# Optimization experiments

Measured on AMD Instinct MI355X. Metric: run time of the kernel, lower is better.

Reference implementation:

```python
import jax, jax.numpy as jnp
import numpy as np

N, B, LMAX, DIM, IMG_DIM, LY, H = 32768, 16, 2560, 512, 768, 256, 8


def _layernorm(x, g, b, eps=1e-5):
    mu = jnp.mean(x, axis=-1, keepdims=True)
    var = jnp.mean(jnp.square(x - mu), axis=-1, keepdims=True)
    return (x - mu) * jax.lax.rsqrt(var + eps) * g + b


def setup_inputs() -> dict:
    key = jax.random.key(0)
    ks = jax.random.split(key, 16)
    s = DIM ** -0.5
    # ragged per-batch counts summing to N, all <= LMAX
    counts = np.full(B, N // B, dtype=np.int64)
    counts[: B // 2] += 200
    counts[B // 2:] -= 200
    batch_ids = jnp.asarray(np.repeat(np.arange(B), counts), dtype=jnp.int32)
    return {
        "F": jax.random.normal(ks[0], (N, DIM), jnp.float32),
        "y": jax.random.normal(ks[1], (B, LY, IMG_DIM), jnp.float32),
        "ln_g": jnp.ones((DIM,), jnp.float32),
        "ln_b": jnp.zeros((DIM,), jnp.float32),
        "Wq": jax.random.normal(ks[2], (DIM, DIM), jnp.float32) * s,
        "Wk": jax.random.normal(ks[3], (DIM, DIM), jnp.float32) * s,
        "Wv": jax.random.normal(ks[4], (DIM, DIM), jnp.float32) * s,
        "bq": jnp.zeros((DIM,), jnp.float32),
        "bk": jnp.zeros((DIM,), jnp.float32),
        "bv": jnp.zeros((DIM,), jnp.float32),
        "Wo": jax.random.normal(ks[5], (DIM, DIM), jnp.float32) * s,
        "bo": jnp.zeros((DIM,), jnp.float32),
        "W1": jax.random.normal(ks[6], (DIM, IMG_DIM), jnp.float32) * (IMG_DIM ** -0.5),
        "b1": jnp.zeros((DIM,), jnp.float32),
        "W2": jax.random.normal(ks[7], (DIM, DIM), jnp.float32) * s,
        "b2": jnp.zeros((DIM,), jnp.float32),
        "batch_ids": batch_ids,
        "Lmax": LMAX,
    }


def reference(F, y, ln_g, ln_b, Wq, Wk, Wv, bq, bk, bv, Wo, bo, W1, b1, W2, b2, batch_ids, Lmax):
    Bb, Ly, _ = y.shape
    n, dim = F.shape
    dh = dim // H
    # sparse -> dense: per-token slot index within its batch (batch_ids sorted)
    offsets = jnp.searchsorted(batch_ids, jnp.arange(Bb, dtype=batch_ids.dtype))
    pos = jnp.arange(n, dtype=jnp.int32) - offsets[batch_ids].astype(jnp.int32)
    xd = jnp.zeros((Bb, Lmax, dim), F.dtype).at[batch_ids, pos].set(F)  # [B,Lmax,D]
    # NOTE: self.norm is re-bound in subclass => same LayerNorm used twice
    xd = _layernorm(xd, ln_g, ln_b)
    # MLP fuse of image features: Linear -> GELU(exact) -> Linear
    ym = jax.nn.gelu(y @ W1.T + b1, approximate=False) @ W2.T + b2  # [B,Ly,D]
    # MHA cross-attention (no key_padding_mask: mask arg defaults to None)
    q = (xd @ Wq.T + bq).reshape(Bb, Lmax, H, dh)
    k = (ym @ Wk.T + bk).reshape(Bb, Ly, H, dh)
    v = (ym @ Wv.T + bv).reshape(Bb, Ly, H, dh)
    scores = jnp.einsum("bqhd,bkhd->bhqk", q, k) * (dh ** -0.5)
    attn = jax.nn.softmax(scores, axis=-1)
    o = jnp.einsum("bhqk,bkhd->bqhd", attn, v).reshape(Bb, Lmax, dim)
    o = o @ Wo.T + bo
    out_dense = _layernorm(xd + o, ln_g, ln_b)
    # dense -> sparse gather (equivalent to x_dense[x_mask])
    return out_dense[batch_ids, pos]
```

## Files before the change

kernel.cpp:

```cpp
#include <hip/hip_runtime.h>
#include <stdint.h>

#define NTOK 32768
#define BD   512
#define NB   16
#define LYK  256
#define IMGD 768

typedef __attribute__((ext_vector_type(4))) float f32x4;
typedef __attribute__((ext_vector_type(8))) short s16x8;
typedef __attribute__((ext_vector_type(4))) unsigned short u16x4;
typedef unsigned short u16;

__device__ __forceinline__ float bf2f(u16 u) {
  union { uint32_t i; float f; } v; v.i = ((uint32_t)u) << 16; return v.f;
}
__device__ __forceinline__ u16 f2bf(float f) {
  union { float f; uint32_t i; } v; v.f = f;
  uint32_t r = v.i + 0x7fffu + ((v.i >> 16) & 1u);
  return (u16)(r >> 16);
}
__device__ __forceinline__ u16 f2bf_fast(float f) {
  union { float f; uint32_t i; } v; v.f = f;
  return (u16)((v.i + 0x8000u) >> 16);
}
__device__ __forceinline__ void gl_lds16(const u16* g, u16* l) {
  __builtin_amdgcn_global_load_lds(
      (const __attribute__((address_space(1))) uint32_t*)g,
      (__attribute__((address_space(3))) uint32_t*)l, 16, 0, 0);
}
__device__ __forceinline__ f32x4 mfma16(s16x8 a, s16x8 b, f32x4 c) {
  return __builtin_amdgcn_mfma_f32_16x16x32_bf16(a, b, c, 0, 0, 0);
}
__device__ __forceinline__ uint32_t cvtpk(float a, float b) {
  uint32_t r;
  asm("v_cvt_pk_bf16_f32 %0, %1, %2" : "=v"(r) : "v"(a), "v"(b));
  return r;
}

__global__ __launch_bounds__(256) void prep(
    const float* __restrict__ wq, const float* __restrict__ wk,
    const float* __restrict__ wv, const float* __restrict__ wo,
    const float* __restrict__ w2, const float* __restrict__ w1,
    const float* __restrict__ y,  const float* __restrict__ F,
    const float* __restrict__ g,  const float* __restrict__ be,
    const int* __restrict__ bids,
    u16* __restrict__ dq, u16* __restrict__ dkv, u16* __restrict__ dwo,
    u16* __restrict__ dw2, u16* __restrict__ dw1, u16* __restrict__ dy,
    u16* __restrict__ xn, int* __restrict__ off) {
  const int bid = blockIdx.x;
  if (bid < 2368) {
    const float* s; u16* d; int base;
    if      (bid < 128)  { s = wq; d = dq;            base = 0;   }
    else if (bid < 256)  { s = wk; d = dkv;           base = 128; }
    else if (bid < 384)  { s = wv; d = dkv + 262144;  base = 256; }
    else if (bid < 512)  { s = wo; d = dwo;           base = 384; }
    else if (bid < 640)  { s = w2; d = dw2;           base = 512; }
    else if (bid < 832)  { s = w1; d = dw1;           base = 640; }
    else                 { s = y;  d = dy;            base = 832; }
    int i = ((bid - base) * 256 + threadIdx.x) * 8;
    f32x4 a = *(const f32x4*)(s + i);
    f32x4 b = *(const f32x4*)(s + i + 4);
    s16x8 o;
#pragma unroll
    for (int j = 0; j < 4; ++j) { o[j] = (short)f2bf(a[j]); o[4 + j] = (short)f2bf(b[j]); }
    *(s16x8*)(d + i) = o;
  } else if (bid < 10560) {
    const int lane = threadIdx.x & 63;
    const size_t row = (size_t)(bid - 2368) * 4 + (threadIdx.x >> 6);
    const float* x = F + row * BD + lane * 8;
    f32x4 a = *(const f32x4*)x;
    f32x4 b = *(const f32x4*)(x + 4);
    float v[8] = {a[0], a[1], a[2], a[3], b[0], b[1], b[2], b[3]};
    float s = 0.f, s2 = 0.f;
#pragma unroll
    for (int j = 0; j < 8; ++j) { s += v[j]; s2 += v[j] * v[j]; }
#pragma unroll
    for (int m = 1; m < 64; m <<= 1) { s += __shfl_xor(s, m); s2 += __shfl_xor(s2, m); }
    float mean = s * (1.f / BD);
    float rstd = rsqrtf(s2 * (1.f / BD) - mean * mean + 1e-5f);
    const float* gp = g + lane * 8;
    const float* bp = be + lane * 8;
    s16x8 o;
#pragma unroll
    for (int j = 0; j < 8; ++j) o[j] = (short)f2bf((v[j] - mean) * rstd * gp[j] + bp[j]);
    *(s16x8*)(xn + row * BD + lane * 8) = o;
  } else {
    int b = threadIdx.x;
    if (b > NB) return;
    int lo = 0, hi = NTOK;
    while (lo < hi) { int mid = (lo + hi) >> 1; if (bids[mid] < b) lo = mid + 1; else hi = mid; }
    off[b] = lo;
  }
}

__global__ __launch_bounds__(256) void ln_bf16_f32(const u16* __restrict__ Z,
                                                   const float* __restrict__ g,
                                                   const float* __restrict__ be,
                                                   float* __restrict__ out) {
  const int lane = threadIdx.x & 63;
  const size_t row = (size_t)blockIdx.x * 4 + (threadIdx.x >> 6);
  s16x8 zv = *(const s16x8*)(Z + row * BD + lane * 8);
  float v[8];
#pragma unroll
  for (int j = 0; j < 8; ++j) v[j] = bf2f((u16)zv[j]);
  float s = 0.f, s2 = 0.f;
#pragma unroll
  for (int j = 0; j < 8; ++j) { s += v[j]; s2 += v[j] * v[j]; }
#pragma unroll
  for (int m = 1; m < 64; m <<= 1) { s += __shfl_xor(s, m); s2 += __shfl_xor(s2, m); }
  float mean = s * (1.f / BD);
  float rstd = rsqrtf(s2 * (1.f / BD) - mean * mean + 1e-5f);
  const float* gp = g + lane * 8;
  const float* bp = be + lane * 8;
  f32x4 o0, o1;
#pragma unroll
  for (int j = 0; j < 4; ++j) o0[j] = (v[j] - mean) * rstd * gp[j] + bp[j];
#pragma unroll
  for (int j = 0; j < 4; ++j) o1[j] = (v[4 + j] - mean) * rstd * gp[4 + j] + bp[4 + j];
  float* op = out + row * BD + lane * 8;
  *(f32x4*)op = o0;
  *(f32x4*)(op + 4) = o1;
}

template <int EPI>
__global__ __launch_bounds__(256, 2) void gemm64(const u16* __restrict__ A,
                                                 const u16* __restrict__ W,
                                                 const float* __restrict__ bias,
                                                 u16* __restrict__ C, int K) {
  __shared__ u16 As[64 * 32];
  __shared__ u16 Bs[128 * 32];
  const int tid = threadIdx.x;
  const int wave = tid >> 6, lane = tid & 63;
  const int wn = wave * 32;
  const int quad = lane >> 4, l16 = lane & 15;
  const int m0 = blockIdx.x * 64, n0 = blockIdx.y * 128;

  f32x4 acc[4][2];
#pragma unroll
  for (int i = 0; i < 4; ++i)
#pragma unroll
    for (int j = 0; j < 2; ++j) acc[i][j] = f32x4{0.f, 0.f, 0.f, 0.f};

  const int scol = (lane & 3) * 8;
  const u16* gA0 = A + (size_t)(m0 + wave * 16 + (lane >> 2)) * K + scol;
  const u16* gW0 = W + (size_t)(n0 + wave * 32 + (lane >> 2)) * K + scol;
  const u16* gW1 = gW0 + (size_t)16 * K;
  u16* lA = As + wave * 512;
  u16* lB = Bs + wave * 1024;

  for (int k0 = 0; k0 < K; k0 += 32) {
    __syncthreads();
    gl_lds16(gA0 + k0, lA);
    gl_lds16(gW0 + k0, lB);
    gl_lds16(gW1 + k0, lB + 512);
    __syncthreads();
    s16x8 af[4], bfr[2];
#pragma unroll
    for (int mt = 0; mt < 4; ++mt)
      af[mt] = *(const s16x8*)&As[(mt * 16 + l16) * 32 + quad * 8];
#pragma unroll
    for (int nt = 0; nt < 2; ++nt)
      bfr[nt] = *(const s16x8*)&Bs[(wn + nt * 16 + l16) * 32 + quad * 8];
#pragma unroll
    for (int mt = 0; mt < 4; ++mt)
#pragma unroll
      for (int nt = 0; nt < 2; ++nt)
        acc[mt][nt] = mfma16(af[mt], bfr[nt], acc[mt][nt]);
  }

#pragma unroll
  for (int nt = 0; nt < 2; ++nt) {
    const int n = n0 + wn + nt * 16 + l16;
    const float bia = bias[n];
#pragma unroll
    for (int mt = 0; mt < 4; ++mt) {
      const int mb = m0 + mt * 16 + quad * 4;
#pragma unroll
      for (int r = 0; r < 4; ++r) {
        float v = acc[mt][nt][r] + bia;
        if (EPI == 1) v = 0.5f * v * (1.f + erff(v * 0.70710678118654752f));
        C[(size_t)(mb + r) * BD + n] = f2bf(v);
      }
    }
  }
}

template <int EPI, int SWZ>
__global__ __launch_bounds__(256, 2) void gemm128(const u16* __restrict__ A,
                                                  const u16* __restrict__ W,
                                                  const float* __restrict__ bias,
                                                  u16* __restrict__ C,
                                                  const u16* __restrict__ resid,
                                                  u16* __restrict__ C2,
                                                  const float* __restrict__ bias2,
                                                  int K) {
  __shared__ u16 As[2][128 * 32];
  __shared__ u16 Bs[2][128 * 32];
  const int tid = threadIdx.x;
  const int wave = tid >> 6, lane = tid & 63;
  const int wm = (wave & 1) * 64, wn = (wave >> 1) * 64;
  const int quad = lane >> 4, l16 = lane & 15;
  int m_t, n_t;
  if (SWZ) {
    const int bid = blockIdx.x;
    const int xcd = bid & 7, j = bid >> 3;
    n_t = j & 3;
    m_t = xcd + (j >> 2) * 8;
  } else {
    m_t = blockIdx.x; n_t = blockIdx.y;
  }
  const int m0 = m_t * 128, n0 = n_t * 128;

  f32x4 acc[4][4];
#pragma unroll
  for (int i = 0; i < 4; ++i)
#pragma unroll
    for (int j = 0; j < 4; ++j) acc[i][j] = f32x4{0.f, 0.f, 0.f, 0.f};

  const int srow = wave * 32 + (lane >> 2);
  const int scol = (lane & 3) * 8;
  const u16* gA0 = A + (size_t)(m0 + srow) * K + scol;
  const u16* gA1 = gA0 + (size_t)16 * K;
  const u16* gW0 = W + (size_t)(n0 + srow) * K + scol;
  const u16* gW1 = gW0 + (size_t)16 * K;
  const int wb = wave * 1024;

  gl_lds16(gA0, &As[0][wb]);
  gl_lds16(gA1, &As[0][wb + 512]);
  gl_lds16(gW0, &Bs[0][wb]);
  gl_lds16(gW1, &Bs[0][wb + 512]);

  int buf = 0;
  for (int k0 = 0; k0 < K; k0 += 32, buf ^= 1) {
    __syncthreads();
    if (k0 + 32 < K) {
      const int nb = buf ^ 1, k1 = k0 + 32;
      gl_lds16(gA0 + k1, &As[nb][wb]);
      gl_lds16(gA1 + k1, &As[nb][wb + 512]);
      gl_lds16(gW0 + k1, &Bs[nb][wb]);
      gl_lds16(gW1 + k1, &Bs[nb][wb + 512]);
    }
    s16x8 af[4], bfr[4];
#pragma unroll
    for (int mt = 0; mt < 4; ++mt)
      af[mt] = *(const s16x8*)&As[buf][(wm + mt * 16 + l16) * 32 + quad * 8];
#pragma unroll
    for (int nt = 0; nt < 4; ++nt)
      bfr[nt] = *(const s16x8*)&Bs[buf][(wn + nt * 16 + l16) * 32 + quad * 8];
#pragma unroll
    for (int mt = 0; mt < 4; ++mt)
#pragma unroll
      for (int nt = 0; nt < 4; ++nt)
        acc[mt][nt] = mfma16(af[mt], bfr[nt], acc[mt][nt]);
  }

#pragma unroll
  for (int nt = 0; nt < 4; ++nt) {
    const int n = n0 + wn + nt * 16 + l16;
    const float bia = (EPI == 3) ? (n < BD ? bias[n] : bias2[n - BD]) : bias[n];
#pragma unroll
    for (int mt = 0; mt < 4; ++mt) {
      const int mb = m0 + wm + mt * 16 + quad * 4;
      if (EPI == 3 && n >= BD) {
        u16x4 pk;
#pragma unroll
        for (int r = 0; r < 4; ++r) pk[r] = f2bf(acc[mt][nt][r] + bia);
        const int b = mb >> 8, k0i = mb & 255;
        *(u16x4*)&C2[((size_t)b * BD + (n - BD)) * LYK + k0i] = pk;
      } else {
#pragma unroll
        for (int r = 0; r < 4; ++r) {
          float v = acc[mt][nt][r] + bia;
          size_t idx = (size_t)(mb + r) * BD + n;
          if (EPI == 2) v += bf2f(resid[idx]);
          C[idx] = f2bf(v);
        }
      }
    }
  }
}

__global__ __launch_bounds__(512, 1) void attn_k(const u16* __restrict__ Q,
                                                 const u16* __restrict__ Kg,
                                                 const u16* __restrict__ VT,
                                                 const int* __restrict__ off,
                                                 u16* __restrict__ O) {
  const int bid = blockIdx.x;
  const int lin = (bid & 7) * 64 + (bid >> 3);
  const int t = lin & 3;
  const int h = (lin >> 2) & 7;
  const int b = lin >> 5;

  __shared__ u16 KS[256 * 64];
  __shared__ u16 VS[64 * 256];
  __shared__ u16 P[128 * 264];

  const int tid = threadIdx.x;
  const int wave = tid >> 6, lane = tid & 63;
  const int quad = lane >> 4, l16 = lane & 15;

  {
    const int c8 = lane & 7, r8 = lane >> 3;
    const u16* kbase = Kg + (size_t)(b * LYK) * BD + h * 64 + ((c8 ^ r8) << 3);
#pragma unroll
    for (int j = 0; j < 4; ++j) {
      const int blk = wave * 4 + j;
      gl_lds16(kbase + (size_t)(blk * 8 + r8) * BD, KS + blk * 512);
    }
    const int c32 = lane & 31, r2 = lane >> 5;
#pragma unroll
    for (int j = 0; j < 4; ++j) {
      const int blk = wave * 4 + j;
      const int r = blk * 2 + r2;
      gl_lds16(VT + (size_t)(b * BD + h * 64 + r) * LYK + ((c32 ^ (r & 31)) << 3),
               VS + blk * 512);
    }
  }
  __syncthreads();

  const int qbase = off[b], qend = off[b + 1];
  const int kc0 = ((quad ^ (l16 & 7)) << 3);
  const int kc1 = (((quad + 4) ^ (l16 & 7)) << 3);
  const int prow = (wave * 16 + l16) * 264;
  int vbase[4], vm[4];
#pragma unroll
  for (int n2 = 0; n2 < 4; ++n2) {
    const int rv = n2 * 16 + l16;
    vbase[n2] = rv * 256;
    vm[n2] = (rv & 31) << 3;
  }

  for (int it = t;; it += 4) {
    const int q0 = qbase + it * 128;
    if (q0 >= qend) break;
    const int qw = q0 + wave * 16;
    if (qw >= qend) continue;
    int qrow = qw + l16;
    if (qrow > qend - 1) qrow = qend - 1;
    const u16* qp = Q + (size_t)qrow * BD + h * 64 + quad * 8;
    const s16x8 aq0 = *(const s16x8*)qp;
    const s16x8 aq1 = *(const s16x8*)(qp + 32);

    f32x4 sacc[16];
#pragma unroll
    for (int nt = 0; nt < 16; ++nt) sacc[nt] = f32x4{0.f, 0.f, 0.f, 0.f};
#pragma unroll
    for (int nt = 0; nt < 16; ++nt) {
      const u16* kp = &KS[(nt * 16 + l16) * 64];
      const s16x8 k0 = *(const s16x8*)(kp + kc0);
      const s16x8 k1 = *(const s16x8*)(kp + kc1);
      sacc[nt] = mfma16(k0, aq0, sacc[nt]);
      sacc[nt] = mfma16(k1, aq1, sacc[nt]);
    }

    f32x4 m4 = sacc[0];
#pragma unroll
    for (int nt = 1; nt < 16; ++nt)
#pragma unroll
      for (int r = 0; r < 4; ++r) m4[r] = fmaxf(m4[r], sacc[nt][r]);
    float mx = fmaxf(fmaxf(m4[0], m4[1]), fmaxf(m4[2], m4[3]));
    mx = fmaxf(mx, __shfl_xor(mx, 16));
    mx = fmaxf(mx, __shfl_xor(mx, 32));
    const float c1 = 0.18033688011112042f;
    const float mc = -mx * c1;
    f32x4 s4 = f32x4{0.f, 0.f, 0.f, 0.f};
#pragma unroll
    for (int nt = 0; nt < 16; ++nt)
#pragma unroll
      for (int r = 0; r < 4; ++r) {
        const float p = __builtin_exp2f(fmaf(sacc[nt][r], c1, mc));
        sacc[nt][r] = p;
        s4[r] += p;
      }
    float sum = (s4[0] + s4[1]) + (s4[2] + s4[3]);
    sum += __shfl_xor(sum, 16);
    sum += __shfl_xor(sum, 32);
    const float inv = 1.f / sum;

#pragma unroll
    for (int nt = 0; nt < 16; ++nt) {
      uint2 pk;
      pk.x = cvtpk(sacc[nt][0], sacc[nt][1]);
      pk.y = cvtpk(sacc[nt][2], sacc[nt][3]);
      *(uint2*)&P[prow + nt * 16 + quad * 4] = pk;
    }

    f32x4 oacc[4];
#pragma unroll
    for (int n2 = 0; n2 < 4; ++n2) oacc[n2] = f32x4{0.f, 0.f, 0.f, 0.f};
#pragma unroll
    for (int kc = 0; kc < 8; ++kc) {
      const s16x8 ap = *(const s16x8*)&P[prow + kc * 32 + quad * 8];
#pragma unroll
      for (int n2 = 0; n2 < 4; ++n2) {
        const s16x8 bv = *(const s16x8*)&VS[vbase[n2] + ((kc * 32 + quad * 8) ^ vm[n2])];
        oacc[n2] = mfma16(ap, bv, oacc[n2]);
      }
    }

    float invr[4];
#pragma unroll
    for (int r = 0; r < 4; ++r) invr[r] = __shfl(inv, quad * 4 + r);
#pragma unroll
    for (int n2 = 0; n2 < 4; ++n2)
#pragma unroll
      for (int r = 0; r < 4; ++r) {
        const int q = qw + quad * 4 + r;
        if (q < qend)
          O[(size_t)q * BD + h * 64 + n2 * 16 + l16] = f2bf(oacc[n2][r] * invr[r]);
      }
  }
}

extern "C" void kernel_launch(void* const* d_in, const int* in_sizes, int n_in,
                              void* d_out, int out_size, void* d_ws, size_t ws_size,
                              hipStream_t stream) {
  const float* F    = (const float*)d_in[0];
  const float* yIn  = (const float*)d_in[1];
  const float* ln_g = (const float*)d_in[2];
  const float* ln_b = (const float*)d_in[3];
  const float* Wq   = (const float*)d_in[4];
  const float* Wk   = (const float*)d_in[5];
  const float* Wv   = (const float*)d_in[6];
  const float* bq   = (const float*)d_in[7];
  const float* bk   = (const float*)d_in[8];
  const float* bv   = (const float*)d_in[9];
  const float* Wo   = (const float*)d_in[10];
  const float* bo   = (const float*)d_in[11];
  const float* W1   = (const float*)d_in[12];
  const float* b1   = (const float*)d_in[13];
  const float* W2   = (const float*)d_in[14];
  const float* b2   = (const float*)d_in[15];
  const int* bids   = (const int*)d_in[16];

  char* ws = (char*)d_ws;
  size_t cur = 0;
  auto alloc = [&](size_t bytes) {
    void* p = ws + cur;
    cur += (bytes + 255) & ~(size_t)255;
    return p;
  };

  int* off   = (int*)alloc(68);
  u16* wq_b  = (u16*)alloc((size_t)262144 * 2);
  u16* wkv_b = (u16*)alloc((size_t)524288 * 2);
  u16* wo_b  = (u16*)alloc((size_t)262144 * 2);
  u16* w2_b  = (u16*)alloc((size_t)262144 * 2);
  u16* w1_b  = (u16*)alloc((size_t)393216 * 2);
  u16* y_b   = (u16*)alloc((size_t)3145728 * 2);
  u16* U     = (u16*)alloc((size_t)4096 * BD * 2);
  u16* ym    = (u16*)alloc((size_t)4096 * BD * 2);
  u16* Kb    = (u16*)alloc((size_t)4096 * BD * 2);
  u16* VT    = (u16*)alloc((size_t)NB * BD * LYK * 2);
  u16* xn    = (u16*)alloc((size_t)NTOK * BD * 2);
  u16* Qb    = (u16*)alloc((size_t)NTOK * BD * 2);
  u16* Ob    = (u16*)alloc((size_t)NTOK * BD * 2);
  u16* Zb    = (u16*)alloc((size_t)NTOK * BD * 2);

  prep<<<10561, 256, 0, stream>>>(Wq, Wk, Wv, Wo, W2, W1, yIn, F, ln_g, ln_b, bids,
                                  wq_b, wkv_b, wo_b, w2_b, w1_b, y_b, xn, off);

  gemm64<1><<<dim3(64, 4), 256, 0, stream>>>(y_b, w1_b, b1, U, IMGD);
  gemm64<0><<<dim3(64, 4), 256, 0, stream>>>(U, w2_b, b2, ym, BD);
  gemm128<3, 0><<<dim3(32, 8), 256, 0, stream>>>(ym, wkv_b, bk, Kb, nullptr, VT, bv, BD);
  gemm128<0, 1><<<1024, 256, 0, stream>>>(xn, wq_b, bq, Qb, nullptr, nullptr, nullptr, BD);
  attn_k<<<512, 512, 0, stream>>>(Qb, Kb, VT, off, Ob);
  gemm128<2, 1><<<1024, 256, 0, stream>>>(Ob, wo_b, bo, Zb, xn, nullptr, nullptr, BD);
  ln_bf16_f32<<<NTOK / 4, 256, 0, stream>>>(Zb, ln_g, ln_b, (float*)d_out);
}
```

Baseline: 339.8 us.

## Keep softmax probabilities in registers via permlane swaps instead of LDS round-trip

```diff
diff --git a/kernel.cpp b/kernel.cpp
--- a/kernel.cpp
+++ b/kernel.cpp
@@ -10,6 +10,7 @@
 typedef __attribute__((ext_vector_type(4))) float f32x4;
 typedef __attribute__((ext_vector_type(8))) short s16x8;
 typedef __attribute__((ext_vector_type(4))) unsigned short u16x4;
+typedef __attribute__((ext_vector_type(4))) int i32x4;
 typedef unsigned short u16;
 
 __device__ __forceinline__ float bf2f(u16 u) {
@@ -19,10 +20,6 @@
   union { float f; uint32_t i; } v; v.f = f;
   uint32_t r = v.i + 0x7fffu + ((v.i >> 16) & 1u);
   return (u16)(r >> 16);
-}
-__device__ __forceinline__ u16 f2bf_fast(float f) {
-  union { float f; uint32_t i; } v; v.f = f;
-  return (u16)((v.i + 0x8000u) >> 16);
 }
 __device__ __forceinline__ void gl_lds16(const u16* g, u16* l) {
   __builtin_amdgcn_global_load_lds(
@@ -281,7 +278,7 @@
   }
 }
 
-__global__ __launch_bounds__(512, 1) void attn_k(const u16* __restrict__ Q,
+__global__ __launch_bounds__(512, 4) void attn_k(const u16* __restrict__ Q,
                                                  const u16* __restrict__ Kg,
                                                  const u16* __restrict__ VT,
                                                  const int* __restrict__ off,
@@ -294,7 +291,6 @@
 
   __shared__ u16 KS[256 * 64];
   __shared__ u16 VS[64 * 256];
-  __shared__ u16 P[128 * 264];
 
   const int tid = threadIdx.x;
   const int wave = tid >> 6, lane = tid & 63;
@@ -322,7 +318,6 @@
   const int qbase = off[b], qend = off[b + 1];
   const int kc0 = ((quad ^ (l16 & 7)) << 3);
   const int kc1 = (((quad + 4) ^ (l16 & 7)) << 3);
-  const int prow = (wave * 16 + l16) * 264;
   int vbase[4], vm[4];
 #pragma unroll
   for (int n2 = 0; n2 < 4; ++n2) {
@@ -364,34 +359,38 @@
     mx = fmaxf(mx, __shfl_xor(mx, 32));
     const float c1 = 0.18033688011112042f;
     const float mc = -mx * c1;
+
     f32x4 s4 = f32x4{0.f, 0.f, 0.f, 0.f};
-#pragma unroll
-    for (int nt = 0; nt < 16; ++nt)
-#pragma unroll
-      for (int r = 0; r < 4; ++r) {
-        const float p = __builtin_exp2f(fmaf(sacc[nt][r], c1, mc));
-        sacc[nt][r] = p;
-        s4[r] += p;
-      }
+    uint32_t pk[32];
+#pragma unroll
+    for (int nt = 0; nt < 16; ++nt) {
+      const float p0 = __builtin_exp2f(fmaf(sacc[nt][0], c1, mc));
+      const float p1 = __builtin_exp2f(fmaf(sacc[nt][1], c1, mc));
+      const float p2 = __builtin_exp2f(fmaf(sacc[nt][2], c1, mc));
+      const float p3 = __builtin_exp2f(fmaf(sacc[nt][3], c1, mc));
+      s4[0] += p0; s4[1] += p1; s4[2] += p2; s4[3] += p3;
+      pk[2 * nt]     = cvtpk(p0, p1);
+      pk[2 * nt + 1] = cvtpk(p2, p3);
+    }
     float sum = (s4[0] + s4[1]) + (s4[2] + s4[3]);
     sum += __shfl_xor(sum, 16);
     sum += __shfl_xor(sum, 32);
     const float inv = 1.f / sum;
 
-#pragma unroll
-    for (int nt = 0; nt < 16; ++nt) {
-      uint2 pk;
-      pk.x = cvtpk(sacc[nt][0], sacc[nt][1]);
-      pk.y = cvtpk(sacc[nt][2], sacc[nt][3]);
-      *(uint2*)&P[prow + nt * 16 + quad * 4] = pk;
-    }
-
     f32x4 oacc[4];
 #pragma unroll
     for (int n2 = 0; n2 < 4; ++n2) oacc[n2] = f32x4{0.f, 0.f, 0.f, 0.f};
 #pragma unroll
     for (int kc = 0; kc < 8; ++kc) {
-      const s16x8 ap = *(const s16x8*)&P[prow + kc * 32 + quad * 8];
+      uint32_t x0 = pk[4 * kc],     y0 = pk[4 * kc + 2];
+      uint32_t x1 = pk[4 * kc + 1], y1 = pk[4 * kc + 3];
+      asm("v_permlane32_swap_b32 %0, %1" : "+v"(x0), "+v"(y0));
+      asm("v_permlane16_swap_b32 %0, %1" : "+v"(x0), "+v"(y0));
+      asm("v_permlane32_swap_b32 %0, %1" : "+v"(x1), "+v"(y1));
+      asm("v_permlane16_swap_b32 %0, %1" : "+v"(x1), "+v"(y1));
+      i32x4 aw;
+      aw[0] = (int)x0; aw[1] = (int)x1; aw[2] = (int)y0; aw[3] = (int)y1;
+      const s16x8 ap = __builtin_bit_cast(s16x8, aw);
 #pragma unroll
       for (int n2 = 0; n2 < 4; ++n2) {
         const s16x8 bv = *(const s16x8*)&VS[vbase[n2] + ((kc * 32 + quad * 8) ^ vm[n2])];
```

Measured after the change: 338.4 us. Within noise of the previous version (-0.4%).

## Rewrite attention kernel with 32x32 MFMA and register-resident probabilities

Applied to the files above, without the earlier changes.

```diff
diff --git a/kernel.cpp b/kernel.cpp
--- a/kernel.cpp
+++ b/kernel.cpp
@@ -8,8 +8,10 @@
 #define IMGD 768
 
 typedef __attribute__((ext_vector_type(4))) float f32x4;
+typedef __attribute__((ext_vector_type(16))) float f32x16;
 typedef __attribute__((ext_vector_type(8))) short s16x8;
 typedef __attribute__((ext_vector_type(4))) unsigned short u16x4;
+typedef __attribute__((ext_vector_type(4))) int i32x4;
 typedef unsigned short u16;
 
 __device__ __forceinline__ float bf2f(u16 u) {
@@ -20,10 +22,6 @@
   uint32_t r = v.i + 0x7fffu + ((v.i >> 16) & 1u);
   return (u16)(r >> 16);
 }
-__device__ __forceinline__ u16 f2bf_fast(float f) {
-  union { float f; uint32_t i; } v; v.f = f;
-  return (u16)((v.i + 0x8000u) >> 16);
-}
 __device__ __forceinline__ void gl_lds16(const u16* g, u16* l) {
   __builtin_amdgcn_global_load_lds(
       (const __attribute__((address_space(1))) uint32_t*)g,
@@ -31,6 +29,9 @@
 }
 __device__ __forceinline__ f32x4 mfma16(s16x8 a, s16x8 b, f32x4 c) {
   return __builtin_amdgcn_mfma_f32_16x16x32_bf16(a, b, c, 0, 0, 0);
+}
+__device__ __forceinline__ f32x16 mfma32(s16x8 a, s16x8 b, f32x16 c) {
+  return __builtin_amdgcn_mfma_f32_32x32x16_bf16(a, b, c, 0, 0, 0);
 }
 __device__ __forceinline__ uint32_t cvtpk(float a, float b) {
   uint32_t r;
@@ -281,37 +282,35 @@
   }
 }
 
-__global__ __launch_bounds__(512, 1) void attn_k(const u16* __restrict__ Q,
+__global__ __launch_bounds__(256, 2) void attn_k(const u16* __restrict__ Q,
                                                  const u16* __restrict__ Kg,
                                                  const u16* __restrict__ VT,
                                                  const int* __restrict__ off,
                                                  u16* __restrict__ O) {
-  const int bid = blockIdx.x;
-  const int lin = (bid & 7) * 64 + (bid >> 3);
-  const int t = lin & 3;
-  const int h = (lin >> 2) & 7;
-  const int b = lin >> 5;
+  const int chunk = blockIdx.x, h = blockIdx.y, b = blockIdx.z;
+  const int qbase = off[b], qend = off[b + 1];
+  const int q0 = qbase + chunk * 128;
+  if (q0 >= qend) return;
 
   __shared__ u16 KS[256 * 64];
   __shared__ u16 VS[64 * 256];
-  __shared__ u16 P[128 * 264];
 
   const int tid = threadIdx.x;
   const int wave = tid >> 6, lane = tid & 63;
-  const int quad = lane >> 4, l16 = lane & 15;
+  const int l32 = lane & 31, hi = lane >> 5;
 
   {
     const int c8 = lane & 7, r8 = lane >> 3;
     const u16* kbase = Kg + (size_t)(b * LYK) * BD + h * 64 + ((c8 ^ r8) << 3);
 #pragma unroll
-    for (int j = 0; j < 4; ++j) {
-      const int blk = wave * 4 + j;
+    for (int j = 0; j < 8; ++j) {
+      const int blk = wave * 8 + j;
       gl_lds16(kbase + (size_t)(blk * 8 + r8) * BD, KS + blk * 512);
     }
     const int c32 = lane & 31, r2 = lane >> 5;
 #pragma unroll
-    for (int j = 0; j < 4; ++j) {
-      const int blk = wave * 4 + j;
+    for (int j = 0; j < 8; ++j) {
+      const int blk = wave * 8 + j;
       const int r = blk * 2 + r2;
       gl_lds16(VT + (size_t)(b * BD + h * 64 + r) * LYK + ((c32 ^ (r & 31)) << 3),
                VS + blk * 512);
@@ -319,97 +318,105 @@
   }
   __syncthreads();
 
-  const int qbase = off[b], qend = off[b + 1];
-  const int kc0 = ((quad ^ (l16 & 7)) << 3);
-  const int kc1 = (((quad + 4) ^ (l16 & 7)) << 3);
-  const int prow = (wave * 16 + l16) * 264;
-  int vbase[4], vm[4];
-#pragma unroll
-  for (int n2 = 0; n2 < 4; ++n2) {
-    const int rv = n2 * 16 + l16;
-    vbase[n2] = rv * 256;
-    vm[n2] = (rv & 31) << 3;
-  }
-
-  for (int it = t;; it += 4) {
-    const int q0 = qbase + it * 128;
-    if (q0 >= qend) break;
-    const int qw = q0 + wave * 16;
-    if (qw >= qend) continue;
-    int qrow = qw + l16;
-    if (qrow > qend - 1) qrow = qend - 1;
-    const u16* qp = Q + (size_t)qrow * BD + h * 64 + quad * 8;
-    const s16x8 aq0 = *(const s16x8*)qp;
-    const s16x8 aq1 = *(const s16x8*)(qp + 32);
-
-    f32x4 sacc[16];
-#pragma unroll
-    for (int nt = 0; nt < 16; ++nt) sacc[nt] = f32x4{0.f, 0.f, 0.f, 0.f};
-#pragma unroll
-    for (int nt = 0; nt < 16; ++nt) {
-      const u16* kp = &KS[(nt * 16 + l16) * 64];
-      const s16x8 k0 = *(const s16x8*)(kp + kc0);
-      const s16x8 k1 = *(const s16x8*)(kp + kc1);
-      sacc[nt] = mfma16(k0, aq0, sacc[nt]);
-      sacc[nt] = mfma16(k1, aq1, sacc[nt]);
-    }
-
-    f32x4 m4 = sacc[0];
-#pragma unroll
-    for (int nt = 1; nt < 16; ++nt)
-#pragma unroll
-      for (int r = 0; r < 4; ++r) m4[r] = fmaxf(m4[r], sacc[nt][r]);
-    float mx = fmaxf(fmaxf(m4[0], m4[1]), fmaxf(m4[2], m4[3]));
-    mx = fmaxf(mx, __shfl_xor(mx, 16));
-    mx = fmaxf(mx, __shfl_xor(mx, 32));
-    const float c1 = 0.18033688011112042f;
-    const float mc = -mx * c1;
-    f32x4 s4 = f32x4{0.f, 0.f, 0.f, 0.f};
-#pragma unroll
-    for (int nt = 0; nt < 16; ++nt)
-#pragma unroll
-      for (int r = 0; r < 4; ++r) {
-        const float p = __builtin_exp2f(fmaf(sacc[nt][r], c1, mc));
-        sacc[nt][r] = p;
-        s4[r] += p;
+  const int qw = q0 + wave * 32;
+  if (qw >= qend) return;
+
+  int qrow = qw + l32;
+  if (qrow > qend - 1) qrow = qend - 1;
+  const u16* qp = Q + (size_t)qrow * BD + h * 64 + hi * 8;
+  s16x8 bq[4];
+#pragma unroll
+  for (int kk = 0; kk < 4; ++kk) bq[kk] = *(const s16x8*)(qp + kk * 16);
+
+  f32x16 sacc[8];
+#pragma unroll
+  for (int kt = 0; kt < 8; ++kt)
+#pragma unroll
+    for (int r = 0; r < 16; ++r) sacc[kt][r] = 0.f;
+#pragma unroll
+  for (int kt = 0; kt < 8; ++kt) {
+    const int krow = kt * 32 + l32;
+    const u16* kp = &KS[krow * 64];
+#pragma unroll
+    for (int kk = 0; kk < 4; ++kk) {
+      const int c = kk * 2 + hi;
+      const s16x8 ka = *(const s16x8*)(kp + ((c ^ (krow & 7)) << 3));
+      sacc[kt] = mfma32(ka, bq[kk], sacc[kt]);
+    }
+  }
+
+  f32x16 m16 = sacc[0];
+#pragma unroll
+  for (int kt = 1; kt < 8; ++kt)
+#pragma unroll
+    for (int r = 0; r < 16; ++r) m16[r] = fmaxf(m16[r], sacc[kt][r]);
+#pragma unroll
+  for (int r = 0; r < 8; ++r) m16[r] = fmaxf(m16[r], m16[r + 8]);
+#pragma unroll
+  for (int r = 0; r < 4; ++r) m16[r] = fmaxf(m16[r], m16[r + 4]);
+  float mx = fmaxf(fmaxf(m16[0], m16[1]), fmaxf(m16[2], m16[3]));
+  mx = fmaxf(mx, __shfl_xor(mx, 32));
+  const float c1 = 0.18033688011112042f;
+  const float mc = -mx * c1;
+
+  f32x16 ssum;
+#pragma unroll
+  for (int r = 0; r < 16; ++r) ssum[r] = 0.f;
+#pragma unroll
+  for (int kt = 0; kt < 8; ++kt)
+#pragma unroll
+    for (int r = 0; r < 16; ++r) {
+      const float p = __builtin_exp2f(fmaf(sacc[kt][r], c1, mc));
+      sacc[kt][r] = p;
+      ssum[r] += p;
+    }
+#pragma unroll
+  for (int r = 0; r < 8; ++r) ssum[r] += ssum[r + 8];
+#pragma unroll
+  for (int r = 0; r < 4; ++r) ssum[r] += ssum[r + 4];
+  float sum = (ssum[0] + ssum[1]) + (ssum[2] + ssum[3]);
+  sum += __shfl_xor(sum, 32);
+  const float inv = 1.f / sum;
+
+  f32x16 oacc0, oacc1;
+#pragma unroll
+  for (int r = 0; r < 16; ++r) { oacc0[r] = 0.f; oacc1[r] = 0.f; }
+#pragma unroll
+  for (int kt = 0; kt < 8; ++kt) {
+    uint32_t pk[8];
+#pragma unroll
+    for (int j = 0; j < 8; ++j)
+      pk[j] = cvtpk(sacc[kt][2 * j] * inv, sacc[kt][2 * j + 1] * inv);
+    asm("v_permlane32_swap_b32 %0, %1" : "+v"(pk[0]), "+v"(pk[2]));
+    asm("v_permlane32_swap_b32 %0, %1" : "+v"(pk[1]), "+v"(pk[3]));
+    asm("v_permlane32_swap_b32 %0, %1" : "+v"(pk[4]), "+v"(pk[6]));
+    asm("v_permlane32_swap_b32 %0, %1" : "+v"(pk[5]), "+v"(pk[7]));
+#pragma unroll
+    for (int kc = 0; kc < 2; ++kc) {
+      i32x4 aw;
+      aw[0] = (int)pk[4 * kc];     aw[1] = (int)pk[4 * kc + 1];
+      aw[2] = (int)pk[4 * kc + 2]; aw[3] = (int)pk[4 * kc + 3];
+      const s16x8 ap = __builtin_bit_cast(s16x8, aw);
+      const int c = kt * 4 + kc * 2 + hi;
+#pragma unroll
+      for (int dt = 0; dt < 2; ++dt) {
+        const int drow = dt * 32 + l32;
+        const s16x8 bv = *(const s16x8*)&VS[drow * 256 + ((c ^ (drow & 31)) << 3)];
+        if (dt == 0) oacc0 = mfma32(ap, bv, oacc0);
+        else         oacc1 = mfma32(ap, bv, oacc1);
       }
-    float sum = (s4[0] + s4[1]) + (s4[2] + s4[3]);
-    sum += __shfl_xor(sum, 16);
-    sum += __shfl_xor(sum, 32);
-    const float inv = 1.f / sum;
-
-#pragma unroll
-    for (int nt = 0; nt < 16; ++nt) {
-      uint2 pk;
-      pk.x = cvtpk(sacc[nt][0], sacc[nt][1]);
-      pk.y = cvtpk(sacc[nt][2], sacc[nt][3]);
-      *(uint2*)&P[prow + nt * 16 + quad * 4] = pk;
-    }
-
-    f32x4 oacc[4];
-#pragma unroll
-    for (int n2 = 0; n2 < 4; ++n2) oacc[n2] = f32x4{0.f, 0.f, 0.f, 0.f};
-#pragma unroll
-    for (int kc = 0; kc < 8; ++kc) {
-      const s16x8 ap = *(const s16x8*)&P[prow + kc * 32 + quad * 8];
-#pragma unroll
-      for (int n2 = 0; n2 < 4; ++n2) {
-        const s16x8 bv = *(const s16x8*)&VS[vbase[n2] + ((kc * 32 + quad * 8) ^ vm[n2])];
-        oacc[n2] = mfma16(ap, bv, oacc[n2]);
-      }
-    }
-
-    float invr[4];
-#pragma unroll
-    for (int r = 0; r < 4; ++r) invr[r] = __shfl(inv, quad * 4 + r);
-#pragma unroll
-    for (int n2 = 0; n2 < 4; ++n2)
-#pragma unroll
-      for (int r = 0; r < 4; ++r) {
-        const int q = qw + quad * 4 + r;
-        if (q < qend)
-          O[(size_t)q * BD + h * 64 + n2 * 16 + l16] = f2bf(oacc[n2][r] * invr[r]);
-      }
+    }
+  }
+
+#pragma unroll
+  for (int r = 0; r < 16; ++r) {
+    const int qv = (r & 3) + 8 * (r >> 2) + 4 * hi;
+    const int q = qw + qv;
+    if (q < qend) {
+      u16* op = O + (size_t)q * BD + h * 64 + l32;
+      op[0]  = f2bf(oacc0[r]);
+      op[32] = f2bf(oacc1[r]);
+    }
   }
 }
 
@@ -465,7 +472,7 @@
   gemm64<0><<<dim3(64, 4), 256, 0, stream>>>(U, w2_b, b2, ym, BD);
   gemm128<3, 0><<<dim3(32, 8), 256, 0, stream>>>(ym, wkv_b, bk, Kb, nullptr, VT, bv, BD);
   gemm128<0, 1><<<1024, 256, 0, stream>>>(xn, wq_b, bq, Qb, nullptr, nullptr, nullptr, BD);
-  attn_k<<<512, 512, 0, stream>>>(Qb, Kb, VT, off, Ob);
+  attn_k<<<dim3(18, 8, NB), 256, 0, stream>>>(Qb, Kb, VT, off, Ob);
   gemm128<2, 1><<<1024, 256, 0, stream>>>(Ob, wo_b, bo, Zb, xn, nullptr, nullptr, BD);
   ln_bf16_f32<<<NTOK / 4, 256, 0, stream>>>(Zb, ln_g, ln_b, (float*)d_out);
 }
```

New measurement: 328.9 us. -3.2%, faster.
